# Performance work log

Measured on AMD Instinct MI355X. Metric: run time of the kernel, lower is better.

Reference implementation:

```python
import jax, jax.numpy as jnp
import numpy as np

NUM_EXPERTS = 16
NUM_K = 2


def setup_inputs() -> dict:
    key = jax.random.key(0)
    k1, k2 = jax.random.split(key)
    x = jax.random.normal(k1, (8, 8192, 1024), dtype=jnp.float32)
    W = jax.random.normal(k2, (NUM_EXPERTS, 1024), dtype=jnp.float32) * (1.0 / np.sqrt(1024))
    b = jnp.zeros((NUM_EXPERTS,), dtype=jnp.float32)
    return {"x": x, "W": W, "b": b}


def reference(x, W, b):
    # logits: [B, S, E]
    logits = jnp.einsum('bsd,ed->bse', x, W) + b
    weights = jax.nn.softmax(logits, axis=-1)
    # top-k over experts, then scatter values back into a sparse gate mask
    topk_vals, topk_idx = jax.lax.top_k(weights, NUM_K)  # [B, S, k]
    # one-hot scatter (E is small, so [B,S,k,E] intermediate is cheap)
    gated = (jax.nn.one_hot(topk_idx, NUM_EXPERTS, dtype=weights.dtype)
             * topk_vals[..., None]).sum(axis=-2)  # [B, S, E]
    # permute(2, 0, 1): [E, B, S]
    return gated.transpose(2, 0, 1), weights.transpose(2, 0, 1)
```

## Files before the change

kernel.cpp:

```cpp
#include <hip/hip_runtime.h>
#include <math.h>


constexpr int D    = 1024;
constexpr int D4   = D / 4;
constexpr int NE   = 16;
constexpr int NTOK = 8 * 8192;
constexpr int TPB  = 256;
constexpr int TOKS = 64;
constexpr int CH4  = 16;
constexpr int NCH  = D4 / CH4;
constexpr int TSTR = CH4 + 1;
constexpr int EPW  = NE / 4;
constexpr int LSTR = NE + 4;

__global__ __launch_bounds__(TPB, 4) void gating_kernel(
    const float* __restrict__ x,
    const float* __restrict__ W,
    const float* __restrict__ bias,
    float* __restrict__ out)
{
    __shared__ float4 tile[2][TOKS * TSTR];
    const int tid  = threadIdx.x;
    const int lane = tid & 63;
    const int wv   = tid >> 6;
    const long blockTok = (long)blockIdx.x * TOKS;

    const int srow = tid >> 4;
    const int scol = tid & 15;
    const float4* __restrict__ xg = (const float4*)x + blockTok * D4;

    const float4* __restrict__ Wq =
        (const float4*)W + (size_t)__builtin_amdgcn_readfirstlane(wv * EPW * D4);

    float4 pf[4];
    #pragma unroll
    for (int s = 0; s < 4; ++s)
        pf[s] = xg[(s * 16 + srow) * D4 + scol];

    float acc[EPW];
    #pragma unroll
    for (int i = 0; i < EPW; ++i) acc[i] = 0.0f;

    #pragma unroll 1
    for (int c = 0; c < NCH; ++c) {
        #pragma unroll
        for (int s = 0; s < 4; ++s)
            tile[c & 1][(s * 16 + srow) * TSTR + scol] = pf[s];
        __syncthreads();
        if (c + 1 < NCH) {
            #pragma unroll
            for (int s = 0; s < 4; ++s)
                pf[s] = xg[(s * 16 + srow) * D4 + (c + 1) * CH4 + scol];
        }
        const float4* __restrict__ row = &tile[c & 1][lane * TSTR];
        #pragma unroll
        for (int j = 0; j < CH4; ++j) {
            const float4 xv = row[j];
            #pragma unroll
            for (int i = 0; i < EPW; ++i) {
                const float4 w4 = Wq[i * D4 + c * CH4 + j];
                acc[i] = fmaf(xv.x, w4.x, acc[i]);
                acc[i] = fmaf(xv.y, w4.y, acc[i]);
                acc[i] = fmaf(xv.z, w4.z, acc[i]);
                acc[i] = fmaf(xv.w, w4.w, acc[i]);
            }
        }
    }

    float* lbuf = (float*)&tile[0][0];
    #pragma unroll
    for (int i = 0; i < EPW; ++i)
        lbuf[lane * LSTR + wv * EPW + i] = acc[i];
    __syncthreads();

    float logits[NE];
    float m = -INFINITY;
    #pragma unroll
    for (int e = 0; e < NE; ++e) {
        logits[e] = lbuf[lane * LSTR + e] + bias[e];
        m = fmaxf(m, logits[e]);
    }
    float w[NE];
    float s = 0.0f;
    #pragma unroll
    for (int e = 0; e < NE; ++e) {
        w[e] = __expf(logits[e] - m);
        s += w[e];
    }
    const float inv = 1.0f / s;
    #pragma unroll
    for (int e = 0; e < NE; ++e) w[e] *= inv;

    float b1 = -1.0f; int i1 = 0;
    float b2 = -1.0f; int i2 = 0;
    #pragma unroll
    for (int e = 0; e < NE; ++e) {
        if (w[e] > b1)      { b2 = b1; i2 = i1; b1 = w[e]; i1 = e; }
        else if (w[e] > b2) { b2 = w[e]; i2 = e; }
    }

    float* __restrict__ out0 = out;
    float* __restrict__ out1 = out + (long)NE * NTOK;
    #pragma unroll
    for (int i = 0; i < EPW; ++i) {
        const int e = wv * EPW + i;
        const float g = (e == i1) ? b1 : ((e == i2) ? b2 : 0.0f);
        out0[(long)e * NTOK + blockTok + lane] = g;
        out1[(long)e * NTOK + blockTok + lane] = w[e];
    }
}

extern "C" void kernel_launch(void* const* d_in, const int* in_sizes, int n_in,
                              void* d_out, int out_size, void* d_ws, size_t ws_size,
                              hipStream_t stream) {
    const float* x = (const float*)d_in[0];
    const float* W = (const float*)d_in[1];
    const float* b = (const float*)d_in[2];
    float* out = (float*)d_out;

    dim3 grid(NTOK / TOKS);
    dim3 block(TPB);
    gating_kernel<<<grid, block, 0, stream>>>(x, W, b, out);
}
```

Baseline: 427.9 us.

## Compute gating logits with bf16x3 split MFMA instead of scalar FP32 FMAs

The FP32 dot-product loop is replaced by MFMA 16x16x32 bf16 instructions. Both x and W are split into three bf16 parts (six cross products) to keep near-FP32 accuracy. A small prep kernel pre-splits W into workspace each call, and x is split on the fly while being staged into double-buffered LDS, with B fragments held in registers. The aim is to relieve the ALU bottleneck so the kernel approaches the memory bound of streaming x, at the cost of extra split arithmetic, more LDS traffic and a second launch.

```diff
diff --git a/kernel.cpp b/kernel.cpp
--- a/kernel.cpp
+++ b/kernel.cpp
@@ -2,112 +2,172 @@
 #include <math.h>
 
 
+typedef __attribute__((ext_vector_type(8))) short frag8;
+typedef __attribute__((ext_vector_type(4))) float f32x4;
+typedef unsigned short u16;
+typedef unsigned int u32;
+
 constexpr int D    = 1024;
-constexpr int D4   = D / 4;
+constexpr int D4   = 256;
 constexpr int NE   = 16;
-constexpr int NTOK = 8 * 8192;
+constexpr int NTOK = 65536;
 constexpr int TPB  = 256;
 constexpr int TOKS = 64;
-constexpr int CH4  = 16;
-constexpr int NCH  = D4 / CH4;
-constexpr int TSTR = CH4 + 1;
-constexpr int EPW  = NE / 4;
-constexpr int LSTR = NE + 4;
+constexpr int NCH  = 16;
+constexpr int RS   = 72;
+constexpr int PL   = TOKS * RS;
+constexpr int LSTR = 20;
 
-__global__ __launch_bounds__(TPB, 4) void gating_kernel(
+__device__ __forceinline__ u16 bf_rne(float v, float* back) {
+    u32 u = __float_as_uint(v);
+    u32 r = (u + 0x7FFFu + ((u >> 16) & 1u)) >> 16;
+    *back = __uint_as_float(r << 16);
+    return (u16)r;
+}
+
+__device__ __forceinline__ void split3(float v, u16& a, u16& b, u16& c) {
+    float t;
+    a = bf_rne(v, &t); float r = v - t;
+    b = bf_rne(r, &t); r -= t;
+    c = bf_rne(r, &t);
+}
+
+__device__ __forceinline__ void loadX(const float4* __restrict__ xg4, int c,
+                                      int tid, float4* pf) {
+    const int col = tid & 15;
+    #pragma unroll
+    for (int s = 0; s < 4; ++s) {
+        const int r = (s << 4) + (tid >> 4);
+        pf[s] = xg4[r * D4 + c * 16 + col];
+    }
+}
+
+__device__ __forceinline__ void loadB(const u16* __restrict__ wb, int c,
+                                      frag8 Bf[2][3]) {
+    #pragma unroll
+    for (int ks = 0; ks < 2; ++ks)
+        #pragma unroll
+        for (int p = 0; p < 3; ++p)
+            Bf[ks][p] = *(const frag8*)(wb + p * (NE * D) + (c * 2 + ks) * 32);
+}
+
+__device__ __forceinline__ void stage(const float4* pf, u16* __restrict__ lbuf,
+                                      int tid) {
+    const int col = tid & 15;
+    #pragma unroll
+    for (int s = 0; s < 4; ++s) {
+        const int r = (s << 4) + (tid >> 4);
+        u16 h[3][4];
+        split3(pf[s].x, h[0][0], h[1][0], h[2][0]);
+        split3(pf[s].y, h[0][1], h[1][1], h[2][1]);
+        split3(pf[s].z, h[0][2], h[1][2], h[2][2]);
+        split3(pf[s].w, h[0][3], h[1][3], h[2][3]);
+        #pragma unroll
+        for (int p = 0; p < 3; ++p) {
+            u32 lo = (u32)h[p][0] | ((u32)h[p][1] << 16);
+            u32 hi = (u32)h[p][2] | ((u32)h[p][3] << 16);
+            *(uint2*)&lbuf[p * PL + r * RS + (col << 2)] = make_uint2(lo, hi);
+        }
+    }
+}
+
+__device__ __forceinline__ void compute(const u16* __restrict__ lbuf,
+                                        const frag8 Bf[2][3],
+                                        int l, int w, f32x4& acc) {
+    const u16* arow = lbuf + (w * 16 + (l & 15)) * RS + (l >> 4) * 8;
+    #pragma unroll
+    for (int ks = 0; ks < 2; ++ks) {
+        frag8 a1 = *(const frag8*)(arow + 0 * PL + ks * 32);
+        frag8 a2 = *(const frag8*)(arow + 1 * PL + ks * 32);
+        frag8 a3 = *(const frag8*)(arow + 2 * PL + ks * 32);
+        acc = __builtin_amdgcn_mfma_f32_16x16x32_bf16(a3, Bf[ks][0], acc, 0, 0, 0);
+        acc = __builtin_amdgcn_mfma_f32_16x16x32_bf16(a2, Bf[ks][1], acc, 0, 0, 0);
+        acc = __builtin_amdgcn_mfma_f32_16x16x32_bf16(a1, Bf[ks][2], acc, 0, 0, 0);
+        acc = __builtin_amdgcn_mfma_f32_16x16x32_bf16(a2, Bf[ks][0], acc, 0, 0, 0);
+        acc = __builtin_amdgcn_mfma_f32_16x16x32_bf16(a1, Bf[ks][1], acc, 0, 0, 0);
+        acc = __builtin_amdgcn_mfma_f32_16x16x32_bf16(a1, Bf[ks][0], acc, 0, 0, 0);
+    }
+}
+
+__global__ void prep_w(const float* __restrict__ W, u16* __restrict__ wsp) {
+    const int i = blockIdx.x * 256 + threadIdx.x;
+    if (i < NE * D) {
+        u16 a, b, c;
+        split3(W[i], a, b, c);
+        wsp[i] = a; wsp[NE * D + i] = b; wsp[2 * NE * D + i] = c;
+    }
+}
+
+__global__ __launch_bounds__(TPB, 2) void gating_mfma(
     const float* __restrict__ x,
-    const float* __restrict__ W,
     const float* __restrict__ bias,
+    const u16* __restrict__ wsp,
     float* __restrict__ out)
 {
-    __shared__ float4 tile[2][TOKS * TSTR];
-    const int tid  = threadIdx.x;
-    const int lane = tid & 63;
-    const int wv   = tid >> 6;
+    __shared__ __align__(16) u16 xls[2 * 3 * PL];
+    const int tid = threadIdx.x;
+    const int l = tid & 63, w = tid >> 6;
     const long blockTok = (long)blockIdx.x * TOKS;
+    const float4* __restrict__ xg4 = (const float4*)x + blockTok * D4;
+    const u16* __restrict__ wb = wsp + (l & 15) * D + (l >> 4) * 8;
 
-    const int srow = tid >> 4;
-    const int scol = tid & 15;
-    const float4* __restrict__ xg = (const float4*)x + blockTok * D4;
-
-    const float4* __restrict__ Wq =
-        (const float4*)W + (size_t)__builtin_amdgcn_readfirstlane(wv * EPW * D4);
-
-    float4 pf[4];
-    #pragma unroll
-    for (int s = 0; s < 4; ++s)
-        pf[s] = xg[(s * 16 + srow) * D4 + scol];
-
-    float acc[EPW];
-    #pragma unroll
-    for (int i = 0; i < EPW; ++i) acc[i] = 0.0f;
+    float4 pfA[4], pfB[4];
+    frag8 BfA[2][3], BfB[2][3];
+    loadX(xg4, 0, tid, pfA);
+    loadB(wb, 0, BfA);
+    f32x4 acc = {0.f, 0.f, 0.f, 0.f};
 
     #pragma unroll 1
-    for (int c = 0; c < NCH; ++c) {
-        #pragma unroll
-        for (int s = 0; s < 4; ++s)
-            tile[c & 1][(s * 16 + srow) * TSTR + scol] = pf[s];
+    for (int c = 0; c < NCH; c += 2) {
+        stage(pfA, xls, tid);
         __syncthreads();
-        if (c + 1 < NCH) {
-            #pragma unroll
-            for (int s = 0; s < 4; ++s)
-                pf[s] = xg[(s * 16 + srow) * D4 + (c + 1) * CH4 + scol];
-        }
-        const float4* __restrict__ row = &tile[c & 1][lane * TSTR];
-        #pragma unroll
-        for (int j = 0; j < CH4; ++j) {
-            const float4 xv = row[j];
-            #pragma unroll
-            for (int i = 0; i < EPW; ++i) {
-                const float4 w4 = Wq[i * D4 + c * CH4 + j];
-                acc[i] = fmaf(xv.x, w4.x, acc[i]);
-                acc[i] = fmaf(xv.y, w4.y, acc[i]);
-                acc[i] = fmaf(xv.z, w4.z, acc[i]);
-                acc[i] = fmaf(xv.w, w4.w, acc[i]);
-            }
-        }
+        loadX(xg4, c + 1, tid, pfB);
+        loadB(wb, c + 1, BfB);
+        compute(xls, BfA, l, w, acc);
+
+        stage(pfB, xls + 3 * PL, tid);
+        __syncthreads();
+        if (c + 2 < NCH) { loadX(xg4, c + 2, tid, pfA); loadB(wb, c + 2, BfA); }
+        compute(xls + 3 * PL, BfB, l, w, acc);
     }
 
-    float* lbuf = (float*)&tile[0][0];
+    float* lb = (float*)xls;
     #pragma unroll
-    for (int i = 0; i < EPW; ++i)
-        lbuf[lane * LSTR + wv * EPW + i] = acc[i];
+    for (int r = 0; r < 4; ++r)
+        lb[(w * 16 + (l >> 4) * 4 + r) * LSTR + (l & 15)] = acc[r];
     __syncthreads();
 
     float logits[NE];
-    float m = -INFINITY;
+    float mx = -INFINITY;
     #pragma unroll
     for (int e = 0; e < NE; ++e) {
-        logits[e] = lbuf[lane * LSTR + e] + bias[e];
-        m = fmaxf(m, logits[e]);
+        logits[e] = lb[l * LSTR + e] + bias[e];
+        mx = fmaxf(mx, logits[e]);
     }
-    float w[NE];
+    float wt[NE];
     float s = 0.0f;
     #pragma unroll
-    for (int e = 0; e < NE; ++e) {
-        w[e] = __expf(logits[e] - m);
-        s += w[e];
-    }
+    for (int e = 0; e < NE; ++e) { wt[e] = __expf(logits[e] - mx); s += wt[e]; }
     const float inv = 1.0f / s;
     #pragma unroll
-    for (int e = 0; e < NE; ++e) w[e] *= inv;
+    for (int e = 0; e < NE; ++e) wt[e] *= inv;
 
     float b1 = -1.0f; int i1 = 0;
     float b2 = -1.0f; int i2 = 0;
     #pragma unroll
     for (int e = 0; e < NE; ++e) {
-        if (w[e] > b1)      { b2 = b1; i2 = i1; b1 = w[e]; i1 = e; }
-        else if (w[e] > b2) { b2 = w[e]; i2 = e; }
+        if (wt[e] > b1)      { b2 = b1; i2 = i1; b1 = wt[e]; i1 = e; }
+        else if (wt[e] > b2) { b2 = wt[e]; i2 = e; }
     }
 
     float* __restrict__ out0 = out;
     float* __restrict__ out1 = out + (long)NE * NTOK;
     #pragma unroll
-    for (int i = 0; i < EPW; ++i) {
-        const int e = wv * EPW + i;
+    for (int i = 0; i < 4; ++i) {
+        const int e = w * 4 + i;
         const float g = (e == i1) ? b1 : ((e == i2) ? b2 : 0.0f);
-        out0[(long)e * NTOK + blockTok + lane] = g;
-        out1[(long)e * NTOK + blockTok + lane] = w[e];
+        out0[(long)e * NTOK + blockTok + l] = g;
+        out1[(long)e * NTOK + blockTok + l] = wt[e];
     }
 }
 
@@ -118,8 +178,8 @@
     const float* W = (const float*)d_in[1];
     const float* b = (const float*)d_in[2];
     float* out = (float*)d_out;
+    u16* wsp = (u16*)d_ws;
 
-    dim3 grid(NTOK / TOKS);
-    dim3 block(TPB);
-    gating_kernel<<<grid, block, 0, stream>>>(x, W, b, out);
+    prep_w<<<64, 256, 0, stream>>>(W, wsp);
+    gating_mfma<<<NTOK / TOKS, TPB, 0, stream>>>(x, b, wsp, out);
 }
```

Result: faster. 381.3 us (-10.9%).
